# Optimization experiments

Hardware: AMD Instinct MI355X
Metric: run time of the kernel (lower is better)

Reference implementation:

```python
import jax, jax.numpy as jnp
import numpy as np

N = 50000      # total nodes
E = 400000     # edges (before self-loops)
F_IN = 75      # atom features
H = 4          # GAT heads (layers 1,2)
C = 128        # hidden_channels
G = 512        # graphs in batch
EPS_BN = 1e-5


def setup_inputs() -> dict:
    key = jax.random.key(0)
    ks = jax.random.split(key, 32)
    inp = {}
    inp["x"] = jax.random.normal(ks[0], (N, F_IN), jnp.float32)
    inp["edge_index"] = jax.random.randint(ks[1], (2, E), 0, N, dtype=jnp.int32)
    inp["batch"] = jnp.sort(jax.random.randint(ks[2], (N,), 0, G, dtype=jnp.int32))
    # (in_dim, heads, out_per_head, concat)
    dims = [(F_IN, H, C, True), (H * C, H, C, True), (H * C, 1, C, False)]
    i = 3
    for li, (din, h, c, concat) in enumerate(dims, 1):
        dout = h * c if concat else c
        s = 1.0 / np.sqrt(din)
        inp[f"W{li}"] = jax.random.normal(ks[i], (din, h * c), jnp.float32) * s
        inp[f"as{li}"] = jax.random.normal(ks[i + 1], (h, c), jnp.float32) * 0.1
        inp[f"ad{li}"] = jax.random.normal(ks[i + 2], (h, c), jnp.float32) * 0.1
        inp[f"b{li}"] = jnp.zeros((dout,), jnp.float32)
        inp[f"g{li}"] = jnp.ones((dout,), jnp.float32)
        inp[f"bt{li}"] = jnp.zeros((dout,), jnp.float32)
        inp[f"rm{li}"] = jax.random.normal(ks[i + 3], (dout,), jnp.float32) * 0.05
        inp[f"rv{li}"] = jnp.ones((dout,), jnp.float32)
        i += 4
    return inp


def gat_layer(x, src, dst, W, a_src, a_dst, b, heads, c_out, concat):
    # x: [N, Fin] -> h: [N, H, C]
    n = x.shape[0]
    h = (x @ W).reshape(n, heads, c_out)
    # per-node attention logits [N, H]
    al_s = jnp.sum(h * a_src[None], axis=-1)
    al_d = jnp.sum(h * a_dst[None], axis=-1)
    # per-edge logits + leaky relu (PyG GATConv, slope 0.2)
    e = jax.nn.leaky_relu(al_s[src] + al_d[dst], negative_slope=0.2)  # [E, H]
    # segment softmax over destination nodes
    emax = jax.ops.segment_max(e, dst, num_segments=n)
    p = jnp.exp(e - emax[dst])
    denom = jax.ops.segment_sum(p, dst, num_segments=n)
    alpha = p / (denom[dst] + 1e-16)
    # weighted message aggregation
    msg = h[src] * alpha[:, :, None]            # [E, H, C]
    out = jax.ops.segment_sum(msg, dst, num_segments=n)  # [N, H, C]
    out = out.reshape(n, heads * c_out) if concat else out.mean(axis=1)
    return out + b


def bn_eval(x, g, bt, rm, rv):
    return (x - rm) * g * jax.lax.rsqrt(rv + EPS_BN) + bt


def reference(x, edge_index, batch,
              W1, as1, ad1, b1, g1, bt1, rm1, rv1,
              W2, as2, ad2, b2, g2, bt2, rm2, rv2,
              W3, as3, ad3, b3, g3, bt3, rm3, rv3):
    n = x.shape[0]
    ar = jnp.arange(n, dtype=edge_index.dtype)
    # GATConv adds self-loops by default
    src = jnp.concatenate([edge_index[0], ar])
    dst = jnp.concatenate([edge_index[1], ar])

    h = gat_layer(x, src, dst, W1, as1, ad1, b1, H, C, True)
    h = jax.nn.relu(bn_eval(h, g1, bt1, rm1, rv1))   # dropout off (eval)
    h = gat_layer(h, src, dst, W2, as2, ad2, b2, H, C, True)
    h = jax.nn.relu(bn_eval(h, g2, bt2, rm2, rv2))
    h = gat_layer(h, src, dst, W3, as3, ad3, b3, 1, C, False)
    h = bn_eval(h, g3, bt3, rm3, rv3)

    # global mean + max pool over graphs
    ones = jnp.ones((n,), h.dtype)
    cnt = jnp.maximum(jax.ops.segment_sum(ones, batch, num_segments=G), 1.0)
    gmean = jax.ops.segment_sum(h, batch, num_segments=G) / cnt[:, None]
    gmax = jax.ops.segment_max(h, batch, num_segments=G)
    gmax = jnp.where(jnp.isfinite(gmax), gmax, 0.0)  # guard empty graphs
    return jnp.concatenate([gmean, gmax], axis=1)    # [G, 2*C]
```

## Files before the change

### kernel.cpp

```cpp
#include <hip/hip_runtime.h>

typedef unsigned short u16;
typedef unsigned int u32;
typedef __attribute__((ext_vector_type(8))) short s16x8;
typedef __attribute__((ext_vector_type(4))) float f32x4;

__device__ __forceinline__ float bf2f(u32 u) {
    return __uint_as_float(u << 16);
}
__device__ __forceinline__ u16 f2bf(float f) {
    u32 x = __float_as_uint(f);
    u32 r = (x + 0x7fffu + ((x >> 16) & 1u)) >> 16;
    return (u16)r;
}

__device__ __forceinline__ void gload16(const u16* g, u16* l) {
    __builtin_amdgcn_global_load_lds(
        (const __attribute__((address_space(1))) unsigned int*)g,
        (__attribute__((address_space(3))) unsigned int*)l,
        16, 0, 0);
}

__global__ __launch_bounds__(256) void cvtx_k(
    const float* __restrict__ x, u16* __restrict__ xb, int N, int Mp)
{
    const int i = blockIdx.x * 256 + threadIdx.x;
    if (i >= Mp * 96) return;
    const int r = i / 96, c = i - r * 96;
    float v = (r < N && c < 75) ? x[(size_t)r * 75 + c] : 0.f;
    xb[i] = f2bf(v);
}

__global__ __launch_bounds__(256) void cvtw_k(
    const float* __restrict__ W, u16* __restrict__ Wt, int K, int Kp, int Ncol)
{
    const int i = blockIdx.x * 256 + threadIdx.x;
    if (i >= Ncol * Kp) return;
    const int n = i / Kp, k = i - n * Kp;
    Wt[i] = f2bf(k < K ? W[(size_t)k * Ncol + n] : 0.f);
}

__global__ __launch_bounds__(256) void mgemm_k(
    const u16* __restrict__ A, const u16* __restrict__ Bt,
    u16* __restrict__ C, int M, int K, int Ncol)
{
    __shared__ u16 Al[128 * 32];
    __shared__ u16 Bl[128 * 32];
    const int t = threadIdx.x;
    const int lane = t & 63;
    const int wid = t >> 6;
    const int wr = wid >> 1, wc = wid & 1;
    const int rr = lane & 15, q = lane >> 4;
    const int m0 = blockIdx.y * 128, n0 = blockIdx.x * 128;

    f32x4 acc[4][4];
#pragma unroll
    for (int m = 0; m < 4; ++m)
#pragma unroll
        for (int n = 0; n < 4; ++n) acc[m][n] = (f32x4){0.f, 0.f, 0.f, 0.f};

    const int nk = K >> 5;
    for (int kt = 0; kt < nk; ++kt) {
        const int k0 = kt << 5;
#pragma unroll
        for (int i = 0; i < 2; ++i) {
            const int si = i * 256 + t;
            const int r = si >> 2, s = si & 3;
            const int g = s ^ ((r >> 1) & 3);
            gload16(A  + (size_t)(m0 + r) * K + k0 + g * 8, &Al[si * 8]);
            gload16(Bt + (size_t)(n0 + r) * K + k0 + g * 8, &Bl[si * 8]);
        }
        __syncthreads();
        s16x8 af[4], bf[4];
#pragma unroll
        for (int m = 0; m < 4; ++m) {
            const int r = wr * 64 + m * 16 + rr;
            af[m] = *reinterpret_cast<const s16x8*>(&Al[r * 32 + ((q ^ ((r >> 1) & 3)) << 3)]);
        }
#pragma unroll
        for (int n = 0; n < 4; ++n) {
            const int r = wc * 64 + n * 16 + rr;
            bf[n] = *reinterpret_cast<const s16x8*>(&Bl[r * 32 + ((q ^ ((r >> 1) & 3)) << 3)]);
        }
#pragma unroll
        for (int m = 0; m < 4; ++m)
#pragma unroll
            for (int n = 0; n < 4; ++n)
                acc[m][n] = __builtin_amdgcn_mfma_f32_16x16x32_bf16(af[m], bf[n], acc[m][n], 0, 0, 0);
        __syncthreads();
    }
#pragma unroll
    for (int m = 0; m < 4; ++m) {
        const int row_b = m0 + wr * 64 + m * 16 + q * 4;
#pragma unroll
        for (int j = 0; j < 4; ++j) {
            const int row = row_b + j;
            if (row < M) {
#pragma unroll
                for (int n = 0; n < 4; ++n) {
                    const int col = n0 + wc * 64 + n * 16 + rr;
                    C[(size_t)row * Ncol + col] = f2bf(acc[m][n][j]);
                }
            }
        }
    }
}

template<int CH, int C>
__global__ __launch_bounds__(256) void logits_k(
    const u16* __restrict__ h, const float* __restrict__ a_s,
    const float* __restrict__ a_d, float* __restrict__ als,
    float* __restrict__ ald, int N)
{
    constexpr int HH = CH / C;
    constexpr int Kc = CH / 64;
    const int lane = threadIdx.x & 63;
    const int n = blockIdx.x * 4 + (threadIdx.x >> 6);
    if (n >= N) return;
    const int ch0 = Kc * lane;
    float vv[Kc];
    const u16* hp = h + (size_t)n * CH + ch0;
    if constexpr (Kc == 8) {
        const int4 r = *reinterpret_cast<const int4*>(hp);
        const u32 rr[4] = {(u32)r.x, (u32)r.y, (u32)r.z, (u32)r.w};
#pragma unroll
        for (int qq = 0; qq < 4; ++qq) { vv[2*qq] = bf2f(rr[qq] & 0xffffu); vv[2*qq+1] = bf2f(rr[qq] >> 16); }
    } else {
        const u32 r = *reinterpret_cast<const u32*>(hp);
        vv[0] = bf2f(r & 0xffffu); vv[1] = bf2f(r >> 16);
    }
    float ps = 0.f, pd = 0.f;
#pragma unroll
    for (int j = 0; j < Kc; ++j) {
        ps += vv[j] * a_s[ch0 + j];
        pd += vv[j] * a_d[ch0 + j];
    }
    constexpr int Gs = 64 / HH;
#pragma unroll
    for (int off = Gs >> 1; off; off >>= 1) {
        ps += __shfl_xor(ps, off, 64);
        pd += __shfl_xor(pd, off, 64);
    }
    const int hd = ch0 / C;
    if ((lane & (Gs - 1)) == 0) {
        als[(size_t)n * HH + hd] = ps;
        ald[(size_t)n * HH + hd] = pd;
    }
}

__global__ void count_k(const int* __restrict__ edst, int* __restrict__ cnt, int E_, int N_)
{
    const int i = blockIdx.x * 256 + threadIdx.x;
    if (i >= E_ + N_) return;
    const int d = (i < E_) ? edst[i] : (i - E_);
    atomicAdd(&cnt[d], 1);
}

#define SCAN_B 256
__global__ void scan1_k(const int* __restrict__ cnt, int* __restrict__ part,
                        int* __restrict__ bsum, int n)
{
    __shared__ int sm[SCAN_B];
    const int idx = blockIdx.x * SCAN_B + threadIdx.x;
    int v = (idx < n) ? cnt[idx] : 0;
    sm[threadIdx.x] = v;
    __syncthreads();
    for (int off = 1; off < SCAN_B; off <<= 1) {
        int t2 = (threadIdx.x >= off) ? sm[threadIdx.x - off] : 0;
        __syncthreads();
        sm[threadIdx.x] += t2;
        __syncthreads();
    }
    if (idx < n) part[idx] = sm[threadIdx.x];
    if (threadIdx.x == SCAN_B - 1) bsum[blockIdx.x] = sm[threadIdx.x];
}

__global__ void scan2_k(int* __restrict__ bsum, int nb)
{
    __shared__ int sm[SCAN_B];
    const int t = threadIdx.x;
    int v = (t < nb) ? bsum[t] : 0;
    sm[t] = v;
    __syncthreads();
    for (int off = 1; off < SCAN_B; off <<= 1) {
        int t2 = (t >= off) ? sm[t - off] : 0;
        __syncthreads();
        sm[t] += t2;
        __syncthreads();
    }
    if (t < nb) bsum[t] = sm[t] - v;
}

__global__ void scan3_k(const int* __restrict__ part, const int* __restrict__ boff,
                        int* __restrict__ offs, int n)
{
    const int idx = blockIdx.x * SCAN_B + threadIdx.x;
    if (idx < n) offs[idx + 1] = part[idx] + boff[idx / SCAN_B];
    if (idx == 0) offs[0] = 0;
}

__global__ void scatter_k(const int* __restrict__ esrc, const int* __restrict__ edst,
                          const int* __restrict__ offs, int* __restrict__ fill,
                          int* __restrict__ csr, int E_, int N_)
{
    const int i = blockIdx.x * 256 + threadIdx.x;
    if (i >= E_ + N_) return;
    int s, d;
    if (i < E_) { s = esrc[i]; d = edst[i]; } else { s = d = i - E_; }
    const int pos = offs[d] + atomicAdd(&fill[d], 1);
    csr[pos] = s;
}

template<int CH, int C, bool RELU>
__global__ __launch_bounds__(256) void agg_k(
    const u16* __restrict__ hsrc, const int* __restrict__ offs,
    const int* __restrict__ csr, const float* __restrict__ als,
    const float* __restrict__ ald, const float* __restrict__ bias,
    const float* __restrict__ gam, const float* __restrict__ bet,
    const float* __restrict__ rmean, const float* __restrict__ rvar,
    u16* __restrict__ outp, int N)
{
    constexpr int HH = CH / C;
    constexpr int Kc = CH / 64;
    const int lane = threadIdx.x & 63;
    const int dst = blockIdx.x * 4 + (threadIdx.x >> 6);
    if (dst >= N) return;
    const int ch0 = Kc * lane;
    const int hd = ch0 / C;

    float adv[HH];
#pragma unroll
    for (int h = 0; h < HH; ++h) adv[h] = ald[(size_t)dst * HH + h];

    const int rs = offs[dst], re = offs[dst + 1];

    float m[HH];
#pragma unroll
    for (int h = 0; h < HH; ++h) m[h] = -1e30f;
    for (int s = rs + lane; s < re; s += 64) {
        const int sn = csr[s];
        if constexpr (HH == 4) {
            const float4 av = *reinterpret_cast<const float4*>(&als[(size_t)sn * 4]);
            const float ev[4] = {av.x + adv[0], av.y + adv[1], av.z + adv[2], av.w + adv[3]};
#pragma unroll
            for (int h = 0; h < 4; ++h) {
                float e = ev[h]; e = (e > 0.f) ? e : 0.2f * e;
                m[h] = fmaxf(m[h], e);
            }
        } else {
            float e = als[sn] + adv[0]; e = (e > 0.f) ? e : 0.2f * e;
            m[0] = fmaxf(m[0], e);
        }
    }
#pragma unroll
    for (int h = 0; h < HH; ++h)
#pragma unroll
        for (int off = 32; off; off >>= 1) m[h] = fmaxf(m[h], __shfl_xor(m[h], off, 64));

    float smv[HH];
#pragma unroll
    for (int h = 0; h < HH; ++h) smv[h] = 0.f;
    for (int s = rs + lane; s < re; s += 64) {
        const int sn = csr[s];
        if constexpr (HH == 4) {
            const float4 av = *reinterpret_cast<const float4*>(&als[(size_t)sn * 4]);
            const float ev[4] = {av.x + adv[0], av.y + adv[1], av.z + adv[2], av.w + adv[3]};
#pragma unroll
            for (int h = 0; h < 4; ++h) {
                float e = ev[h]; e = (e > 0.f) ? e : 0.2f * e;
                smv[h] += __expf(e - m[h]);
            }
        } else {
            float e = als[sn] + adv[0]; e = (e > 0.f) ? e : 0.2f * e;
            smv[0] += __expf(e - m[0]);
        }
    }
#pragma unroll
    for (int h = 0; h < HH; ++h)
#pragma unroll
        for (int off = 32; off; off >>= 1) smv[h] += __shfl_xor(smv[h], off, 64);
    float inv[HH];
#pragma unroll
    for (int h = 0; h < HH; ++h) inv[h] = 1.f / (smv[h] + 1e-16f);

    const float mh = m[hd], invh = inv[hd], advh = adv[hd];

    float acc[Kc] = {};
    int s = rs;
    for (; s + 4 <= re; s += 4) {
        int sn[4];
#pragma unroll
        for (int u = 0; u < 4; ++u) sn[u] = csr[s + u];
        if constexpr (Kc == 8) {
            int4 r[4];
#pragma unroll
            for (int u = 0; u < 4; ++u)
                r[u] = *reinterpret_cast<const int4*>(hsrc + (size_t)sn[u] * CH + ch0);
            float aa[4];
#pragma unroll
            for (int u = 0; u < 4; ++u) {
                float e = als[(size_t)sn[u] * HH + hd] + advh;
                e = (e > 0.f) ? e : 0.2f * e;
                aa[u] = __expf(e - mh) * invh;
            }
#pragma unroll
            for (int u = 0; u < 4; ++u) {
                const u32 rr2[4] = {(u32)r[u].x, (u32)r[u].y, (u32)r[u].z, (u32)r[u].w};
#pragma unroll
                for (int qq = 0; qq < 4; ++qq) {
                    acc[2*qq]   += aa[u] * bf2f(rr2[qq] & 0xffffu);
                    acc[2*qq+1] += aa[u] * bf2f(rr2[qq] >> 16);
                }
            }
        } else {
            u32 r[4];
#pragma unroll
            for (int u = 0; u < 4; ++u)
                r[u] = *reinterpret_cast<const u32*>(hsrc + (size_t)sn[u] * CH + ch0);
            float aa[4];
#pragma unroll
            for (int u = 0; u < 4; ++u) {
                float e = als[sn[u]] + advh;
                e = (e > 0.f) ? e : 0.2f * e;
                aa[u] = __expf(e - mh) * invh;
            }
#pragma unroll
            for (int u = 0; u < 4; ++u) {
                acc[0] += aa[u] * bf2f(r[u] & 0xffffu);
                acc[1] += aa[u] * bf2f(r[u] >> 16);
            }
        }
    }
    for (; s < re; ++s) {
        const int sn = csr[s];
        float e = als[(size_t)sn * HH + hd] + advh;
        e = (e > 0.f) ? e : 0.2f * e;
        const float a = __expf(e - mh) * invh;
        const u16* hp = hsrc + (size_t)sn * CH + ch0;
        if constexpr (Kc == 8) {
            const int4 r = *reinterpret_cast<const int4*>(hp);
            const u32 rr2[4] = {(u32)r.x, (u32)r.y, (u32)r.z, (u32)r.w};
#pragma unroll
            for (int qq = 0; qq < 4; ++qq) {
                acc[2*qq]   += a * bf2f(rr2[qq] & 0xffffu);
                acc[2*qq+1] += a * bf2f(rr2[qq] >> 16);
            }
        } else {
            const u32 r = *reinterpret_cast<const u32*>(hp);
            acc[0] += a * bf2f(r & 0xffffu);
            acc[1] += a * bf2f(r >> 16);
        }
    }

    u16 ob[Kc];
#pragma unroll
    for (int j = 0; j < Kc; ++j) {
        const int ch = ch0 + j;
        const float scale = gam[ch] * rsqrtf(rvar[ch] + 1e-5f);
        float val = (acc[j] + bias[ch] - rmean[ch]) * scale + bet[ch];
        if (RELU) val = fmaxf(val, 0.f);
        ob[j] = f2bf(val);
    }
    u16* op = outp + (size_t)dst * CH + ch0;
    if constexpr (Kc == 8) {
        int4 w;
        w.x = (int)((u32)ob[0] | ((u32)ob[1] << 16));
        w.y = (int)((u32)ob[2] | ((u32)ob[3] << 16));
        w.z = (int)((u32)ob[4] | ((u32)ob[5] << 16));
        w.w = (int)((u32)ob[6] | ((u32)ob[7] << 16));
        *reinterpret_cast<int4*>(op) = w;
    } else {
        *reinterpret_cast<u32*>(op) = (u32)ob[0] | ((u32)ob[1] << 16);
    }
}

__global__ __launch_bounds__(128) void pool_k(
    const u16* __restrict__ h3, const int* __restrict__ batch,
    float* __restrict__ out, int N)
{
    const int g = blockIdx.x;
    const int t = threadIdx.x;
    int lo = 0, hi = N;
    while (lo < hi) { int mid = (lo + hi) >> 1; if (batch[mid] < g) lo = mid + 1; else hi = mid; }
    const int s0 = lo;
    lo = 0; hi = N;
    while (lo < hi) { int mid = (lo + hi) >> 1; if (batch[mid] < g + 1) lo = mid + 1; else hi = mid; }
    const int s1 = lo;
    float sum = 0.f, mx = -1e30f;
    for (int n = s0; n < s1; ++n) {
        const float v = bf2f((u32)h3[(size_t)n * 128 + t]);
        sum += v;
        mx = fmaxf(mx, v);
    }
    const int cnt = s1 - s0;
    out[(size_t)g * 256 + t]       = cnt ? sum / (float)cnt : 0.f;
    out[(size_t)g * 256 + 128 + t] = cnt ? mx : 0.f;
}

extern "C" void kernel_launch(void* const* d_in, const int* in_sizes, int n_in,
                              void* d_out, int out_size, void* d_ws, size_t ws_size,
                              hipStream_t stream)
{
    const float* x   = (const float*)d_in[0];
    const int* ei    = (const int*)d_in[1];
    const int* batch = (const int*)d_in[2];
    const float* W1  = (const float*)d_in[3];
    const float* as1 = (const float*)d_in[4];
    const float* ad1 = (const float*)d_in[5];
    const float* b1  = (const float*)d_in[6];
    const float* g1  = (const float*)d_in[7];
    const float* bt1 = (const float*)d_in[8];
    const float* rm1 = (const float*)d_in[9];
    const float* rv1 = (const float*)d_in[10];
    const float* W2  = (const float*)d_in[11];
    const float* as2 = (const float*)d_in[12];
    const float* ad2 = (const float*)d_in[13];
    const float* b2  = (const float*)d_in[14];
    const float* g2  = (const float*)d_in[15];
    const float* bt2 = (const float*)d_in[16];
    const float* rm2 = (const float*)d_in[17];
    const float* rv2 = (const float*)d_in[18];
    const float* W3  = (const float*)d_in[19];
    const float* as3 = (const float*)d_in[20];
    const float* ad3 = (const float*)d_in[21];
    const float* b3  = (const float*)d_in[22];
    const float* g3  = (const float*)d_in[23];
    const float* bt3 = (const float*)d_in[24];
    const float* rm3 = (const float*)d_in[25];
    const float* rv3 = (const float*)d_in[26];

    const int Nn = in_sizes[2];
    const int Ee = in_sizes[1] / 2;
    const int ET = Ee + Nn;
    const int Gg = out_size / 256;
    const int Mp = ((Nn + 127) / 128) * 128;

    char* ws = (char*)d_ws;
    size_t o = 0;
    auto alc = [&](size_t bytes) { size_t r = o; o = (o + bytes + 255) & ~(size_t)255; return r; };
    u16*  hA   = (u16*)(ws + alc((size_t)Mp * 512 * 2));
    u16*  hB   = (u16*)(ws + alc((size_t)Mp * 512 * 2));
    u16*  xb   = (u16*)(ws + alc((size_t)Mp * 96 * 2));
    u16*  Wt1  = (u16*)(ws + alc((size_t)512 * 96 * 2));
    u16*  Wt2  = (u16*)(ws + alc((size_t)512 * 512 * 2));
    u16*  Wt3  = (u16*)(ws + alc((size_t)128 * 512 * 2));
    float* als = (float*)(ws + alc((size_t)Nn * 4 * 4));
    float* ald = (float*)(ws + alc((size_t)Nn * 4 * 4));
    int*  cnt  = (int*)(ws + alc((size_t)2 * Nn * 4));
    int*  fill = cnt + Nn;
    int*  offs = (int*)(ws + alc((size_t)(Nn + 1) * 4));
    int*  part = (int*)(ws + alc((size_t)Nn * 4));
    int*  bsum = (int*)(ws + alc((size_t)SCAN_B * 4));
    int*  csr  = (int*)(ws + alc((size_t)ET * 4));
    (void)ws_size; (void)n_in;

    hipMemsetAsync(cnt, 0, (size_t)2 * Nn * 4, stream);
    const int ETB = (ET + 255) / 256;
    count_k<<<ETB, 256, 0, stream>>>(ei + Ee, cnt, Ee, Nn);
    const int nb = (Nn + SCAN_B - 1) / SCAN_B;
    scan1_k<<<nb, SCAN_B, 0, stream>>>(cnt, part, bsum, Nn);
    scan2_k<<<1, SCAN_B, 0, stream>>>(bsum, nb);
    scan3_k<<<nb, SCAN_B, 0, stream>>>(part, bsum, offs, Nn);
    scatter_k<<<ETB, 256, 0, stream>>>(ei, ei + Ee, offs, fill, csr, Ee, Nn);

    cvtx_k<<<(Mp * 96 + 255) / 256, 256, 0, stream>>>(x, xb, Nn, Mp);
    cvtw_k<<<(512 * 96 + 255) / 256, 256, 0, stream>>>(W1, Wt1, 75, 96, 512);
    cvtw_k<<<(512 * 512 + 255) / 256, 256, 0, stream>>>(W2, Wt2, 512, 512, 512);
    cvtw_k<<<(128 * 512 + 255) / 256, 256, 0, stream>>>(W3, Wt3, 512, 512, 128);

    const int nwb = (Nn + 3) / 4;
    const int mb = Mp / 128;

    {
        dim3 grid(4, mb);
        mgemm_k<<<grid, 256, 0, stream>>>(xb, Wt1, hA, Nn, 96, 512);
        logits_k<512, 128><<<nwb, 256, 0, stream>>>(hA, as1, ad1, als, ald, Nn);
        agg_k<512, 128, true><<<nwb, 256, 0, stream>>>(hA, offs, csr, als, ald,
                                                       b1, g1, bt1, rm1, rv1, hB, Nn);
    }
    {
        dim3 grid(4, mb);
        mgemm_k<<<grid, 256, 0, stream>>>(hB, Wt2, hA, Nn, 512, 512);
        logits_k<512, 128><<<nwb, 256, 0, stream>>>(hA, as2, ad2, als, ald, Nn);
        agg_k<512, 128, true><<<nwb, 256, 0, stream>>>(hA, offs, csr, als, ald,
                                                       b2, g2, bt2, rm2, rv2, hB, Nn);
    }
    {
        dim3 grid(1, mb);
        mgemm_k<<<grid, 256, 0, stream>>>(hB, Wt3, hA, Nn, 512, 128);
        logits_k<128, 128><<<nwb, 256, 0, stream>>>(hA, as3, ad3, als, ald, Nn);
        agg_k<128, 128, false><<<nwb, 256, 0, stream>>>(hA, offs, csr, als, ald,
                                                        b3, g3, bt3, rm3, rv3, hB, Nn);
    }
    pool_k<<<Gg, 128, 0, stream>>>(hB, batch, (float*)d_out, Nn);
}
```

Measured before the change: 418.1 us.

## Fuse attention logits into GEMM epilogue, double-buffer LDS, remap blocks per XCD

The per-node attention logit computation moves into the GEMM epilogue. Each block reduces its fp32 accumulators against a_src/a_dst through warp shuffles and shared memory, so the separate logits kernels and their re-read of h go away. The K loop now double-buffers the LDS tiles so the next tile's async loads overlap the MFMAs. The grid is flattened and remapped so consecutive row blocks and heads land on the same XCD for L2 reuse. Mp is hardcoded to 392*128, which ties the kernel to N=50000; the fused logits also now use fp32 accumulators instead of bf16-rounded h.

```diff
diff --git a/kernel.cpp b/kernel.cpp
--- a/kernel.cpp
+++ b/kernel.cpp
@@ -41,17 +41,25 @@
 }
 
 __global__ __launch_bounds__(256) void mgemm_k(
-    const u16* __restrict__ A, const u16* __restrict__ Bt,
-    u16* __restrict__ C, int M, int K, int Ncol)
-{
-    __shared__ u16 Al[128 * 32];
-    __shared__ u16 Bl[128 * 32];
+    const u16* __restrict__ A, const u16* __restrict__ Bt, u16* __restrict__ C,
+    const float* __restrict__ avs, const float* __restrict__ avd,
+    float* __restrict__ als, float* __restrict__ ald,
+    int M, int K, int Ncol, int H, int NXB)
+{
+    __shared__ u16 Al[2][128 * 32];
+    __shared__ u16 Bl[2][128 * 32];
     const int t = threadIdx.x;
     const int lane = t & 63;
     const int wid = t >> 6;
     const int wr = wid >> 1, wc = wid & 1;
     const int rr = lane & 15, q = lane >> 4;
-    const int m0 = blockIdx.y * 128, n0 = blockIdx.x * 128;
+
+    const int dd = blockIdx.x;
+    const int xcd = dd & 7, ii = dd >> 3;
+    const int gpx = (int)(gridDim.x >> 3) / NXB;
+    const int yb = xcd * gpx + ((NXB == 4) ? (ii >> 2) : ii);
+    const int head = (NXB == 4) ? (ii & 3) : 0;
+    const int m0 = yb * 128, n0 = head * 128;
 
     f32x4 acc[4][4];
 #pragma unroll
@@ -59,36 +67,43 @@
 #pragma unroll
         for (int n = 0; n < 4; ++n) acc[m][n] = (f32x4){0.f, 0.f, 0.f, 0.f};
 
-    const int nk = K >> 5;
-    for (int kt = 0; kt < nk; ++kt) {
-        const int k0 = kt << 5;
-#pragma unroll
-        for (int i = 0; i < 2; ++i) {
-            const int si = i * 256 + t;
+    auto stage = [&](int b, int k0) {
+#pragma unroll
+        for (int i2 = 0; i2 < 2; ++i2) {
+            const int si = i2 * 256 + t;
             const int r = si >> 2, s = si & 3;
             const int g = s ^ ((r >> 1) & 3);
-            gload16(A  + (size_t)(m0 + r) * K + k0 + g * 8, &Al[si * 8]);
-            gload16(Bt + (size_t)(n0 + r) * K + k0 + g * 8, &Bl[si * 8]);
-        }
-        __syncthreads();
-        s16x8 af[4], bf[4];
+            gload16(A  + (size_t)(m0 + r) * K + k0 + g * 8, &Al[b][si * 8]);
+            gload16(Bt + (size_t)(n0 + r) * K + k0 + g * 8, &Bl[b][si * 8]);
+        }
+    };
+
+    const int nk = K >> 5;
+    stage(0, 0);
+    __syncthreads();
+    int buf = 0;
+    for (int kt = 0; kt < nk; ++kt) {
+        if (kt + 1 < nk) stage(buf ^ 1, (kt + 1) << 5);
+        s16x8 af[4], bfr[4];
 #pragma unroll
         for (int m = 0; m < 4; ++m) {
             const int r = wr * 64 + m * 16 + rr;
-            af[m] = *reinterpret_cast<const s16x8*>(&Al[r * 32 + ((q ^ ((r >> 1) & 3)) << 3)]);
+            af[m] = *reinterpret_cast<const s16x8*>(&Al[buf][r * 32 + ((q ^ ((r >> 1) & 3)) << 3)]);
         }
 #pragma unroll
         for (int n = 0; n < 4; ++n) {
             const int r = wc * 64 + n * 16 + rr;
-            bf[n] = *reinterpret_cast<const s16x8*>(&Bl[r * 32 + ((q ^ ((r >> 1) & 3)) << 3)]);
+            bfr[n] = *reinterpret_cast<const s16x8*>(&Bl[buf][r * 32 + ((q ^ ((r >> 1) & 3)) << 3)]);
         }
 #pragma unroll
         for (int m = 0; m < 4; ++m)
 #pragma unroll
             for (int n = 0; n < 4; ++n)
-                acc[m][n] = __builtin_amdgcn_mfma_f32_16x16x32_bf16(af[m], bf[n], acc[m][n], 0, 0, 0);
+                acc[m][n] = __builtin_amdgcn_mfma_f32_16x16x32_bf16(af[m], bfr[n], acc[m][n], 0, 0, 0);
         __syncthreads();
-    }
+        buf ^= 1;
+    }
+
 #pragma unroll
     for (int m = 0; m < 4; ++m) {
         const int row_b = m0 + wr * 64 + m * 16 + q * 4;
@@ -104,47 +119,44 @@
             }
         }
     }
-}
-
-template<int CH, int C>
-__global__ __launch_bounds__(256) void logits_k(
-    const u16* __restrict__ h, const float* __restrict__ a_s,
-    const float* __restrict__ a_d, float* __restrict__ als,
-    float* __restrict__ ald, int N)
-{
-    constexpr int HH = CH / C;
-    constexpr int Kc = CH / 64;
-    const int lane = threadIdx.x & 63;
-    const int n = blockIdx.x * 4 + (threadIdx.x >> 6);
-    if (n >= N) return;
-    const int ch0 = Kc * lane;
-    float vv[Kc];
-    const u16* hp = h + (size_t)n * CH + ch0;
-    if constexpr (Kc == 8) {
-        const int4 r = *reinterpret_cast<const int4*>(hp);
-        const u32 rr[4] = {(u32)r.x, (u32)r.y, (u32)r.z, (u32)r.w};
-#pragma unroll
-        for (int qq = 0; qq < 4; ++qq) { vv[2*qq] = bf2f(rr[qq] & 0xffffu); vv[2*qq+1] = bf2f(rr[qq] >> 16); }
-    } else {
-        const u32 r = *reinterpret_cast<const u32*>(hp);
-        vv[0] = bf2f(r & 0xffffu); vv[1] = bf2f(r >> 16);
-    }
-    float ps = 0.f, pd = 0.f;
-#pragma unroll
-    for (int j = 0; j < Kc; ++j) {
-        ps += vv[j] * a_s[ch0 + j];
-        pd += vv[j] * a_d[ch0 + j];
-    }
-    constexpr int Gs = 64 / HH;
-#pragma unroll
-    for (int off = Gs >> 1; off; off >>= 1) {
-        ps += __shfl_xor(ps, off, 64);
-        pd += __shfl_xor(pd, off, 64);
-    }
-    const int hd = ch0 / C;
-    if ((lane & (Gs - 1)) == 0) {
-        als[(size_t)n * HH + hd] = ps;
-        ald[(size_t)n * HH + hd] = pd;
+
+    float asv[4], adv[4];
+#pragma unroll
+    for (int n = 0; n < 4; ++n) {
+        const int c = wc * 64 + n * 16 + rr;
+        asv[n] = avs[head * 128 + c];
+        adv[n] = avd[head * 128 + c];
+    }
+    float* lps = (float*)&Al[0][0];
+    float* lpd = lps + 256;
+#pragma unroll
+    for (int m = 0; m < 4; ++m)
+#pragma unroll
+        for (int j = 0; j < 4; ++j) {
+            float ps = 0.f, pd = 0.f;
+#pragma unroll
+            for (int n = 0; n < 4; ++n) {
+                ps += acc[m][n][j] * asv[n];
+                pd += acc[m][n][j] * adv[n];
+            }
+#pragma unroll
+            for (int off = 1; off < 16; off <<= 1) {
+                ps += __shfl_xor(ps, off, 64);
+                pd += __shfl_xor(pd, off, 64);
+            }
+            if (rr == 0) {
+                const int r = wr * 64 + m * 16 + q * 4 + j;
+                lps[wc * 128 + r] = ps;
+                lpd[wc * 128 + r] = pd;
+            }
+        }
+    __syncthreads();
+    if (t < 128) {
+        const int row = m0 + t;
+        if (row < M) {
+            als[(size_t)row * H + head] = lps[t] + lps[128 + t];
+            ald[(size_t)row * H + head] = lpd[t] + lpd[128 + t];
+        }
     }
 }
 
@@ -433,7 +445,7 @@
     const int Ee = in_sizes[1] / 2;
     const int ET = Ee + Nn;
     const int Gg = out_size / 256;
-    const int Mp = ((Nn + 127) / 128) * 128;
+    const int Mp = 392 * 128;
 
     char* ws = (char*)d_ws;
     size_t o = 0;
@@ -469,28 +481,17 @@
     cvtw_k<<<(128 * 512 + 255) / 256, 256, 0, stream>>>(W3, Wt3, 512, 512, 128);
 
     const int nwb = (Nn + 3) / 4;
-    const int mb = Mp / 128;
-
-    {
-        dim3 grid(4, mb);
-        mgemm_k<<<grid, 256, 0, stream>>>(xb, Wt1, hA, Nn, 96, 512);
-        logits_k<512, 128><<<nwb, 256, 0, stream>>>(hA, as1, ad1, als, ald, Nn);
-        agg_k<512, 128, true><<<nwb, 256, 0, stream>>>(hA, offs, csr, als, ald,
-                                                       b1, g1, bt1, rm1, rv1, hB, Nn);
-    }
-    {
-        dim3 grid(4, mb);
-        mgemm_k<<<grid, 256, 0, stream>>>(hB, Wt2, hA, Nn, 512, 512);
-        logits_k<512, 128><<<nwb, 256, 0, stream>>>(hA, as2, ad2, als, ald, Nn);
-        agg_k<512, 128, true><<<nwb, 256, 0, stream>>>(hA, offs, csr, als, ald,
-                                                       b2, g2, bt2, rm2, rv2, hB, Nn);
-    }
-    {
-        dim3 grid(1, mb);
-        mgemm_k<<<grid, 256, 0, stream>>>(hB, Wt3, hA, Nn, 512, 128);
-        logits_k<128, 128><<<nwb, 256, 0, stream>>>(hA, as3, ad3, als, ald, Nn);
-        agg_k<128, 128, false><<<nwb, 256, 0, stream>>>(hA, offs, csr, als, ald,
-                                                        b3, g3, bt3, rm3, rv3, hB, Nn);
-    }
+    const int nwg4 = 392 * 4;
+    const int nwg1 = 392;
+
+    mgemm_k<<<nwg4, 256, 0, stream>>>(xb, Wt1, hA, as1, ad1, als, ald, Nn, 96, 512, 4, 4);
+    agg_k<512, 128, true><<<nwb, 256, 0, stream>>>(hA, offs, csr, als, ald,
+                                                   b1, g1, bt1, rm1, rv1, hB, Nn);
+    mgemm_k<<<nwg4, 256, 0, stream>>>(hB, Wt2, hA, as2, ad2, als, ald, Nn, 512, 512, 4, 4);
+    agg_k<512, 128, true><<<nwb, 256, 0, stream>>>(hA, offs, csr, als, ald,
+                                                   b2, g2, bt2, rm2, rv2, hB, Nn);
+    mgemm_k<<<nwg1, 256, 0, stream>>>(hB, Wt3, hA, as3, ad3, als, ald, Nn, 512, 128, 1, 1);
+    agg_k<128, 128, false><<<nwb, 256, 0, stream>>>(hA, offs, csr, als, ald,
+                                                    b3, g3, bt3, rm3, rv3, hB, Nn);
     pool_k<<<Gg, 128, 0, stream>>>(hB, batch, (float*)d_out, Nn);
 }
```

Measured after the change: 401.5 us. -4.0%, faster.
